# Optimization experiments

Measured on AMD Instinct MI355X. Metric: run time of the kernel, lower is better.

## Reference

```python
import jax, jax.numpy as jnp
import numpy as np

N, M, A, O, F = 4, 64, 64, 5, 256


def _sph_harm_l2(R):
    # real spherical harmonics up to l=2 (9 components) of the unit direction
    r = jnp.linalg.norm(R, axis=-1, keepdims=True)
    u = R / (r + 1e-12)
    x, y, z = u[..., 0], u[..., 1], u[..., 2]
    c1 = 0.4886025119029199
    c2 = 1.0925484305920792
    return jnp.stack([
        jnp.full_like(x, 0.28209479177387814),
        c1 * y, c1 * z, c1 * x,
        c2 * x * y, c2 * y * z,
        0.31539156525252005 * (3.0 * z * z - 1.0),
        c2 * x * z,
        0.5462742152960396 * (x * x - y * y),
    ], axis=-1)  # [..., 9]


def setup_inputs() -> dict:
    key = jax.random.key(0)
    ks = jax.random.split(key, 6)
    return {
        "ao_embeddings": jax.random.normal(ks[0], (N, M, A, O, F), jnp.float32),
        "C": jax.random.normal(ks[1], (N, M, A, O), jnp.float32),
        "S": jax.random.normal(ks[2], (N, A, 3, A, 3), jnp.float32),
        "R": jax.random.normal(ks[3], (N, M, A, 3), jnp.float32),
        "w_stack": jax.random.normal(ks[4], (5, 3, 3), jnp.float32) * 0.5,
        "cgc": jax.random.normal(ks[5], (9, 9, 9), jnp.float32) * 0.1,
    }


def reference(ao_embeddings, C, S, R, w_stack, cgc):
    # mo_features: [n, m, a, o=5, f]
    mo = C[..., None] * ao_embeddings
    # 5-step bilinear transform of the overlap-like tensor S [n, a, 3, b, 3]
    Sc = S
    for i in range(5):
        w = w_stack[i]  # [3, 3]
        Sc = jnp.einsum('ab,cd,kibjd->kiajc', w, w, Sc)
        Sc = jax.nn.swish(Sc)
    filt = jnp.array([[1., 1., 0.], [1., 1., 0.], [0., 0., 1.]], Sc.dtype)
    Sc = filt[None, None, :, None, :] * Sc
    idx = jnp.array([0, 1, 2, 2, 2])  # tf.repeat(repeats=[1, 1, 3]) -> size 5
    Sc = jnp.take(jnp.take(Sc, idx, axis=2), idx, axis=4)  # [n, a, 5, b, 5]
    # message passing over atom pairs: [n, m, b, p=5, f]
    mo = jnp.einsum('nmaof,naobp->nmbpf', mo, Sc)
    # unsorted_segment_sum with segment_ids [0,0,1,2,3] into 9 slots == matmul with one-hot map
    seg = jnp.zeros((5, 9), mo.dtype).at[jnp.arange(5), jnp.array([0, 0, 1, 2, 3])].set(1.0)
    mo = jnp.einsum('nmbpf,pq->nmbqf', mo, seg)  # [n, m, a, 9, f]
    # coupling: sph harmonics * ||C|| (tf.repeat over f == broadcast, folded into einsum)
    Cn = jnp.linalg.norm(C, axis=-1)            # [n, m, a]
    coup = _sph_harm_l2(R) * Cn[..., None]      # [n, m, a, 9]
    # CG contraction + sum over atoms a: [n, m, i=9, f]
    out = jnp.einsum('nmapf,nmak,kip->nmif', mo, coup, cgc)
    return jnp.transpose(out, (0, 1, 3, 2))     # [n, m, f, 9]
```

## Files before the change

kernel.cpp:

```cpp
#include <hip/hip_runtime.h>
#include <math.h>


__global__ void k_sc(const float* __restrict__ S, const float* __restrict__ wst,
                     float* __restrict__ G) {
    int t = blockIdx.x * 256 + threadIdx.x;
    int n = t >> 12;
    int a = (t >> 6) & 63;
    int b = t & 63;
    float M[3][3];
#pragma unroll
    for (int x = 0; x < 3; ++x)
#pragma unroll
        for (int y = 0; y < 3; ++y)
            M[x][y] = S[(((n * 64 + a) * 3 + x) * 64 + b) * 3 + y];
#pragma unroll
    for (int it = 0; it < 5; ++it) {
        float w[3][3];
#pragma unroll
        for (int x = 0; x < 3; ++x)
#pragma unroll
            for (int y = 0; y < 3; ++y)
                w[x][y] = wst[it * 9 + x * 3 + y];
        float T[3][3];
#pragma unroll
        for (int x = 0; x < 3; ++x)
#pragma unroll
            for (int d = 0; d < 3; ++d)
                T[x][d] = w[x][0] * M[0][d] + w[x][1] * M[1][d] + w[x][2] * M[2][d];
#pragma unroll
        for (int x = 0; x < 3; ++x)
#pragma unroll
            for (int c = 0; c < 3; ++c) {
                float v = T[x][0] * w[c][0] + T[x][1] * w[c][1] + T[x][2] * w[c][2];
                M[x][c] = v / (1.f + expf(-v));
            }
    }
    float g0 = M[0][0] + M[0][1];
    float g1 = M[1][0] + M[1][1];
    float gz = M[2][2];
    size_t base = (size_t)n * 12288 + (size_t)b * 64 + a;
    G[base]          = g0;
    G[base + 4096]   = g1;
    G[base + 8192]   = gz;
}

__global__ __launch_bounds__(512) void k_w3(
        const float* __restrict__ C, const float* __restrict__ R,
        const float* __restrict__ cgc, const float* __restrict__ G,
        float* __restrict__ coeff) {
    __shared__ float s_coup[64 * 9];
    __shared__ float s_D[2 * 9 * 64];
    __shared__ float s_W3[64 * 3 * 9];

    const int nm = blockIdx.x;
    const int n = nm >> 6;
    const int tid = threadIdx.x;

    if (tid < 64) {
        const int b = tid;
        const float* rp = R + ((size_t)nm * 64 + b) * 3;
        float x = rp[0], y = rp[1], z = rp[2];
        float rn = sqrtf(x * x + y * y + z * z) + 1e-12f;
        x /= rn; y /= rn; z /= rn;
        const float* cp = C + ((size_t)nm * 64 + b) * 5;
        float cn = 0.f;
#pragma unroll
        for (int o = 0; o < 5; ++o) cn += cp[o] * cp[o];
        cn = sqrtf(cn);
        const float c1 = 0.4886025119029199f;
        const float c2 = 1.0925484305920792f;
        float Y[9];
        Y[0] = 0.28209479177387814f;
        Y[1] = c1 * y;
        Y[2] = c1 * z;
        Y[3] = c1 * x;
        Y[4] = c2 * x * y;
        Y[5] = c2 * y * z;
        Y[6] = 0.31539156525252005f * (3.f * z * z - 1.f);
        Y[7] = c2 * x * z;
        Y[8] = 0.5462742152960396f * (x * x - y * y);
#pragma unroll
        for (int k = 0; k < 9; ++k) s_coup[b * 9 + k] = Y[k] * cn;
    }
    __syncthreads();

    for (int e = tid; e < 576; e += 512) {
        const int b = e & 63, i = e >> 6;
        float d0 = 0.f, dz = 0.f;
#pragma unroll
        for (int k = 0; k < 9; ++k) {
            float cp = s_coup[b * 9 + k];
            const float* cg = cgc + k * 81 + i * 9;
            d0 = fmaf(cp, cg[0], d0);
            dz = fmaf(cp, cg[1] + cg[2] + cg[3], dz);
        }
        s_D[(0 * 9 + i) * 64 + b] = d0;
        s_D[(1 * 9 + i) * 64 + b] = dz;
    }
    __syncthreads();

    const int wid = __builtin_amdgcn_readfirstlane(tid >> 6);
    const int lane = tid & 63;
    for (int pp = wid; pp < 9; pp += 8) {
        const int u = pp / 3;
        const int i0 = (pp % 3) * 3;
        const int pm = (u == 2) ? 1 : 0;
        const float* gp = G + (size_t)n * 12288 + (size_t)u * 4096 + lane;
        const float* dp = &s_D[(pm * 9 + i0) * 64];
        float a0 = 0.f, a1 = 0.f, a2 = 0.f;
#pragma unroll 8
        for (int b = 0; b < 64; ++b) {
            float g = gp[b * 64];
            a0 = fmaf(g, dp[b], a0);
            a1 = fmaf(g, dp[64 + b], a1);
            a2 = fmaf(g, dp[128 + b], a2);
        }
        s_W3[(lane * 3 + u) * 9 + i0 + 0] = a0;
        s_W3[(lane * 3 + u) * 9 + i0 + 1] = a1;
        s_W3[(lane * 3 + u) * 9 + i0 + 2] = a2;
    }
    __syncthreads();

    const float* Cb = C + (size_t)nm * 320;
    float* cf = coeff + (size_t)nm * 320 * 9;
    for (int e = tid; e < 2880; e += 512) {
        int a = e / 45;
        int rem = e - a * 45;
        int o = rem / 9;
        int i = rem - o * 9;
        int u = o < 2 ? o : 2;
        cf[e] = Cb[a * 5 + o] * s_W3[(a * 3 + u) * 9 + i];
    }
}

__global__ __launch_bounds__(512) void k_out(
        const float* __restrict__ ao, const float* __restrict__ coeff,
        float* __restrict__ out) {
    __shared__ float s_red[3 * 128 * 9];
    const int bid = blockIdx.x;
    const int nm = bid >> 1;
    const int fh = bid & 1;
    const int tid = threadIdx.x;
    const int fl = tid & 127;
    const int f = fh * 128 + fl;
    const int rq = __builtin_amdgcn_readfirstlane(tid >> 7);
    const int rbase = rq * 80;
    const float* ap = ao + ((size_t)nm * 320 + rbase) * 256 + f;
    const float* cf = coeff + ((size_t)nm * 320 + rbase) * 9;
    float acc[9];
#pragma unroll
    for (int i = 0; i < 9; ++i) acc[i] = 0.f;
#pragma unroll 8
    for (int r = 0; r < 80; ++r) {
        float v = ap[(size_t)r * 256];
#pragma unroll
        for (int i = 0; i < 9; ++i) acc[i] = fmaf(cf[r * 9 + i], v, acc[i]);
    }
    if (rq > 0) {
        float* sp = &s_red[((rq - 1) * 128 + fl) * 9];
#pragma unroll
        for (int i = 0; i < 9; ++i) sp[i] = acc[i];
    }
    __syncthreads();
    if (rq == 0) {
        float* op = out + ((size_t)nm * 256 + f) * 9;
#pragma unroll
        for (int i = 0; i < 9; ++i)
            op[i] = acc[i] + s_red[(0 * 128 + fl) * 9 + i]
                           + s_red[(1 * 128 + fl) * 9 + i]
                           + s_red[(2 * 128 + fl) * 9 + i];
    }
}

extern "C" void kernel_launch(void* const* d_in, const int* in_sizes, int n_in,
                              void* d_out, int out_size, void* d_ws, size_t ws_size,
                              hipStream_t stream) {
    (void)in_sizes; (void)n_in; (void)out_size; (void)ws_size;
    const float* ao  = (const float*)d_in[0];
    const float* C   = (const float*)d_in[1];
    const float* S   = (const float*)d_in[2];
    const float* R   = (const float*)d_in[3];
    const float* wst = (const float*)d_in[4];
    const float* cgc = (const float*)d_in[5];
    float* out = (float*)d_out;
    float* ws = (float*)d_ws;
    float* G     = ws;
    float* coeff = ws + 49152;

    hipLaunchKernelGGL(k_sc,  dim3(64),  dim3(256), 0, stream, S, wst, G);
    hipLaunchKernelGGL(k_w3,  dim3(256), dim3(512), 0, stream, C, R, cgc, G, coeff);
    hipLaunchKernelGGL(k_out, dim3(512), dim3(512), 0, stream, ao, coeff, out);
}
```

Measured before the change: 33.92 us.

## Rework k_out reduction with float2 loads and 8-way wave split; resize k_sc/k_w3 launches

k_out now has each lane handle two adjacent features through float2 loads. The 320 rows are split across 8 waves of 40 rows each, and the partials are reduced through shared memory with coalesced output writes. This is meant to raise memory-level parallelism on the dominant ao stream and make the final stores contiguous, at the cost of more shared memory. k_w3 is launched with 576 threads so each of the 9 work groups gets its own wave, removing the tail loop iteration. k_sc uses 128 blocks of 128 threads to spread work over more CUs.

```diff
diff --git a/kernel.cpp b/kernel.cpp
--- a/kernel.cpp
+++ b/kernel.cpp
@@ -4,7 +4,7 @@
 
 __global__ void k_sc(const float* __restrict__ S, const float* __restrict__ wst,
                      float* __restrict__ G) {
-    int t = blockIdx.x * 256 + threadIdx.x;
+    int t = blockIdx.x * 128 + threadIdx.x;
     int n = t >> 12;
     int a = (t >> 6) & 63;
     int b = t & 63;
@@ -45,7 +45,7 @@
     G[base + 8192]   = gz;
 }
 
-__global__ __launch_bounds__(512) void k_w3(
+__global__ __launch_bounds__(576) void k_w3(
         const float* __restrict__ C, const float* __restrict__ R,
         const float* __restrict__ cgc, const float* __restrict__ G,
         float* __restrict__ coeff) {
@@ -85,8 +85,8 @@
     }
     __syncthreads();
 
-    for (int e = tid; e < 576; e += 512) {
-        const int b = e & 63, i = e >> 6;
+    {
+        const int b = tid & 63, i = tid >> 6;
         float d0 = 0.f, dz = 0.f;
 #pragma unroll
         for (int k = 0; k < 9; ++k) {
@@ -100,9 +100,9 @@
     }
     __syncthreads();
 
-    const int wid = __builtin_amdgcn_readfirstlane(tid >> 6);
+    const int pp = __builtin_amdgcn_readfirstlane(tid >> 6);
     const int lane = tid & 63;
-    for (int pp = wid; pp < 9; pp += 8) {
+    {
         const int u = pp / 3;
         const int i0 = (pp % 3) * 3;
         const int pm = (u == 2) ? 1 : 0;
@@ -124,7 +124,7 @@
 
     const float* Cb = C + (size_t)nm * 320;
     float* cf = coeff + (size_t)nm * 320 * 9;
-    for (int e = tid; e < 2880; e += 512) {
+    for (int e = tid; e < 2880; e += 576) {
         int a = e / 45;
         int rem = e - a * 45;
         int o = rem / 9;
@@ -137,39 +137,40 @@
 __global__ __launch_bounds__(512) void k_out(
         const float* __restrict__ ao, const float* __restrict__ coeff,
         float* __restrict__ out) {
-    __shared__ float s_red[3 * 128 * 9];
+    __shared__ float s_par[8][128 * 9];
     const int bid = blockIdx.x;
     const int nm = bid >> 1;
     const int fh = bid & 1;
     const int tid = threadIdx.x;
-    const int fl = tid & 127;
-    const int f = fh * 128 + fl;
-    const int rq = __builtin_amdgcn_readfirstlane(tid >> 7);
-    const int rbase = rq * 80;
-    const float* ap = ao + ((size_t)nm * 320 + rbase) * 256 + f;
+    const int lane = tid & 63;
+    const int w = __builtin_amdgcn_readfirstlane(tid >> 6);
+    const int rbase = w * 40;
+    const float* ap = ao + ((size_t)nm * 320 + rbase) * 256 + fh * 128 + lane * 2;
     const float* cf = coeff + ((size_t)nm * 320 + rbase) * 9;
-    float acc[9];
+    float acc[9][2];
 #pragma unroll
-    for (int i = 0; i < 9; ++i) acc[i] = 0.f;
+    for (int i = 0; i < 9; ++i) { acc[i][0] = 0.f; acc[i][1] = 0.f; }
 #pragma unroll 8
-    for (int r = 0; r < 80; ++r) {
-        float v = ap[(size_t)r * 256];
+    for (int r = 0; r < 40; ++r) {
+        float2 v = *reinterpret_cast<const float2*>(ap + (size_t)r * 256);
 #pragma unroll
-        for (int i = 0; i < 9; ++i) acc[i] = fmaf(cf[r * 9 + i], v, acc[i]);
+        for (int i = 0; i < 9; ++i) {
+            float c = cf[r * 9 + i];
+            acc[i][0] = fmaf(c, v.x, acc[i][0]);
+            acc[i][1] = fmaf(c, v.y, acc[i][1]);
+        }
     }
-    if (rq > 0) {
-        float* sp = &s_red[((rq - 1) * 128 + fl) * 9];
 #pragma unroll
-        for (int i = 0; i < 9; ++i) sp[i] = acc[i];
-    }
-    __syncthreads();
-    if (rq == 0) {
-        float* op = out + ((size_t)nm * 256 + f) * 9;
+    for (int j = 0; j < 2; ++j)
 #pragma unroll
         for (int i = 0; i < 9; ++i)
-            op[i] = acc[i] + s_red[(0 * 128 + fl) * 9 + i]
-                           + s_red[(1 * 128 + fl) * 9 + i]
-                           + s_red[(2 * 128 + fl) * 9 + i];
+            s_par[w][(lane * 2 + j) * 9 + i] = acc[i][j];
+    __syncthreads();
+    for (int s = tid; s < 1152; s += 512) {
+        float sum = 0.f;
+#pragma unroll
+        for (int w2 = 0; w2 < 8; ++w2) sum += s_par[w2][s];
+        out[(size_t)nm * 2304 + fh * 1152 + s] = sum;
     }
 }
 
@@ -188,7 +189,7 @@
     float* G     = ws;
     float* coeff = ws + 49152;
 
-    hipLaunchKernelGGL(k_sc,  dim3(64),  dim3(256), 0, stream, S, wst, G);
-    hipLaunchKernelGGL(k_w3,  dim3(256), dim3(512), 0, stream, C, R, cgc, G, coeff);
+    hipLaunchKernelGGL(k_sc,  dim3(128), dim3(128), 0, stream, S, wst, G);
+    hipLaunchKernelGGL(k_w3,  dim3(256), dim3(576), 0, stream, C, R, cgc, G, coeff);
     hipLaunchKernelGGL(k_out, dim3(512), dim3(512), 0, stream, ao, coeff, out);
 }
```

Result: no change. 33.67 us (-0.7%).
